# Kernel optimization log

Hardware: AMD Instinct MI355X
Metric: run time of the kernel (lower is better)

Reference implementation:

```python
import jax, jax.numpy as jnp
import numpy as np

IN_DIM, H1, H2, H3, LATENT = 1024, 1024, 512, 256, 256
D, K, BETA = 32, 2048, 0.25
B = 16384


def _leaky(x):
    return jax.nn.leaky_relu(x, negative_slope=0.01)


def setup_inputs() -> dict:
    key = jax.random.key(0)
    ks = jax.random.split(key, 18)
    def lin(k, fan_in, fan_out):
        kw, kb = jax.random.split(k)
        s = 1.0 / np.sqrt(fan_in)
        W = jax.random.uniform(kw, (fan_in, fan_out), jnp.float32, -s, s)
        b = jax.random.uniform(kb, (fan_out,), jnp.float32, -s, s)
        return W, b
    We1, be1 = lin(ks[0], IN_DIM, H1)
    We2, be2 = lin(ks[1], H1, H2)
    We3, be3 = lin(ks[2], H2, H3)
    We4, be4 = lin(ks[3], H3, LATENT)
    Wd1, bd1 = lin(ks[4], LATENT, H3)
    Wd2, bd2 = lin(ks[5], H3, H2)
    Wd3, bd3 = lin(ks[6], H2, H1)
    Wd4, bd4 = lin(ks[7], H1, IN_DIM)
    E = jax.random.uniform(ks[8], (K, D), jnp.float32, -1.0 / K, 1.0 / K)  # codebook
    x = jax.random.uniform(ks[9], (B, IN_DIM), jnp.float32)
    return {"x": x, "We1": We1, "be1": be1, "We2": We2, "be2": be2,
            "We3": We3, "be3": be3, "We4": We4, "be4": be4, "E": E,
            "Wd1": Wd1, "bd1": bd1, "Wd2": Wd2, "bd2": bd2,
            "Wd3": Wd3, "bd3": bd3, "Wd4": Wd4, "bd4": bd4}


def reference(x, We1, be1, We2, be2, We3, be3, We4, be4, E,
              Wd1, bd1, Wd2, bd2, Wd3, bd3, Wd4, bd4):
    # encoder MLP
    h = _leaky(x @ We1 + be1)
    h = _leaky(h @ We2 + be2)
    h = _leaky(h @ We3 + be3)
    z = h @ We4 + be4                      # [B, LATENT]
    # vector quantizer
    zr = z.reshape(-1, D)                  # [N, D], N = B*LATENT/D
    dist = (jnp.sum(zr * zr, axis=1, keepdims=True)
            + jnp.sum(E * E, axis=1)
            - 2.0 * zr @ E.T)              # [N, K]
    idx = jnp.argmin(dist, axis=1)         # [N]
    # one-hot @ E == direct gather of nearest codebook rows
    q = E[idx].reshape(z.shape)            # [B, LATENT]
    commit = jnp.mean(jnp.sum(jnp.square(jax.lax.stop_gradient(q) - z), axis=1))
    embed = jnp.mean(jnp.sum(jnp.square(q - jax.lax.stop_gradient(z)), axis=1))
    vq_loss = BETA * commit + embed
    e = z + jax.lax.stop_gradient(q - z)   # straight-through
    # decoder MLP
    h = _leaky(e @ Wd1 + bd1)
    h = _leaky(h @ Wd2 + bd2)
    h = _leaky(h @ Wd3 + bd3)
    recon = jax.nn.sigmoid(h @ Wd4 + bd4)
    recon_loss = jnp.mean(jnp.sum(jnp.square(recon - x), axis=-1))
    loss = recon_loss + vq_loss
    return z, e, recon, loss, recon_loss, vq_loss
```

## Files before the change

kernel.cpp:

```cpp
#include <hip/hip_runtime.h>
#include <stdint.h>

typedef __attribute__((ext_vector_type(8))) _Float16 half8;
typedef __attribute__((ext_vector_type(4))) _Float16 half4;
typedef __attribute__((ext_vector_type(4))) float f32x4;

__device__ __forceinline__ void gload_lds16(const void* g, void* l) {
  __builtin_amdgcn_global_load_lds(
      (const __attribute__((address_space(1))) void*)g,
      (__attribute__((address_space(3))) void*)l, 16, 0, 0);
}

template <int EPI, int BM, int BN>
__global__ __launch_bounds__(256, (BM == 128 ? 2 : 4)) void gemm_bt(
    const _Float16* __restrict__ A, const _Float16* __restrict__ Bt,
    const float* __restrict__ bias, _Float16* __restrict__ Ch,
    float* __restrict__ Cf, int M, int N, int Kd,
    const float* __restrict__ Xref, float* __restrict__ lossAcc) {
  constexpr int WM = BM / 2, WN = BN / 2;
  constexpr int MF = WM / 16, NF = WN / 16;
  constexpr int CA = BM / 32, CB = BN / 32;
  constexpr int SMEMH = ((BN * 128) > ((BM + BN) * 64)) ? (BN * 128)
                                                        : ((BM + BN) * 64);
  __shared__ __align__(16) _Float16 smem[SMEMH];
  __shared__ float red[256];
  _Float16* As = smem;
  _Float16* Bs = smem + BM * 64;

  const int tid = threadIdx.x;
  const int lane = tid & 63;
  const int wav = tid >> 6;
  const int m0 = blockIdx.y * BM;
  const int n0 = blockIdx.x * BN;
  const int wm = (wav >> 1) * WM;
  const int wn = (wav & 1) * WN;
  const int l15 = lane & 15;
  const int quad = lane >> 4;

  f32x4 acc[MF][NF];
#pragma unroll
  for (int i = 0; i < MF; i++)
#pragma unroll
    for (int j = 0; j < NF; j++) acc[i][j] = (f32x4){0.f, 0.f, 0.f, 0.f};

  for (int kt = 0; kt < Kd; kt += 64) {
    __syncthreads();
#pragma unroll
    for (int j = 0; j < CA; j++) {
      const int ci = j * 256 + tid;
      const int row = ci >> 3;
      const int kc = ((ci & 7) ^ (row & 7)) << 3;
      gload_lds16(A + (size_t)(m0 + row) * Kd + kt + kc, &As[ci * 8]);
    }
#pragma unroll
    for (int j = 0; j < CB; j++) {
      const int ci = j * 256 + tid;
      const int row = ci >> 3;
      const int kc = ((ci & 7) ^ (row & 7)) << 3;
      gload_lds16(Bt + (size_t)(n0 + row) * Kd + kt + kc, &Bs[ci * 8]);
    }
    __syncthreads();

#pragma unroll
    for (int s = 0; s < 2; s++) {
      half8 af[MF], bq[NF];
#pragma unroll
      for (int i = 0; i < MF; i++) {
        const int ra = wm + i * 16 + l15;
        const int ca = (s * 4 + quad) ^ (ra & 7);
        af[i] = *(const half8*)&As[ra * 64 + ca * 8];
      }
#pragma unroll
      for (int i = 0; i < NF; i++) {
        const int rb = wn + i * 16 + l15;
        const int cb = (s * 4 + quad) ^ (rb & 7);
        bq[i] = *(const half8*)&Bs[rb * 64 + cb * 8];
      }
#pragma unroll
      for (int mi = 0; mi < MF; mi++)
#pragma unroll
        for (int ni = 0; ni < NF; ni++)
          acc[mi][ni] = __builtin_amdgcn_mfma_f32_16x16x32_f16(af[mi], bq[ni],
                                                               acc[mi][ni], 0, 0, 0);
    }
  }

  float lsum = 0.f;
  float* eb = (float*)smem;
  constexpr int DIV = BN / 4;
#pragma unroll
  for (int p = 0; p < BM / 64; p++) {
    __syncthreads();
    if ((wm >> 6) == p) {
#pragma unroll
      for (int mi = 0; mi < MF; mi++)
#pragma unroll
        for (int ni = 0; ni < NF; ni++)
#pragma unroll
          for (int r = 0; r < 4; r++) {
            const int rl = (wm & 63) + mi * 16 + quad * 4 + r;
            const int cl = wn + ni * 16 + l15;
            eb[rl * BN + cl] = acc[mi][ni][r];
          }
    }
    __syncthreads();
#pragma unroll
    for (int j = 0; j < BN / 16; j++) {
      const int c = j * 256 + tid;
      const int rl = c / DIV;
      const int cl = (c % DIV) * 4;
      const f32x4 v = *(const f32x4*)&eb[rl * BN + cl];
      const int gcol = n0 + cl;
      const f32x4 bv = *(const f32x4*)&bias[gcol];
      const size_t o = (size_t)(m0 + p * 64 + rl) * N + gcol;
      if (EPI == 0) {
        half4 h;
#pragma unroll
        for (int q = 0; q < 4; q++) {
          float t = v[q] + bv[q];
          t = t > 0.f ? t : 0.01f * t;
          h[q] = (_Float16)t;
        }
        *(half4*)&Ch[o] = h;
      } else if (EPI == 1) {
        f32x4 t;
        half4 h;
#pragma unroll
        for (int q = 0; q < 4; q++) {
          t[q] = v[q] + bv[q];
          h[q] = (_Float16)t[q];
        }
        *(f32x4*)&Cf[o] = t;
        *(half4*)&Ch[o] = h;
      } else {
        const f32x4 xr = *(const f32x4*)&Xref[o];
        f32x4 sv;
#pragma unroll
        for (int q = 0; q < 4; q++) {
          const float s = 1.f / (1.f + __expf(-(v[q] + bv[q])));
          sv[q] = s;
          const float d = s - xr[q];
          lsum += d * d;
        }
        *(f32x4*)&Cf[o] = sv;
      }
    }
  }
  if (EPI == 2) {
    __syncthreads();
    red[tid] = lsum;
    __syncthreads();
    for (int s = 128; s > 0; s >>= 1) {
      if (tid < s) red[tid] += red[tid + s];
      __syncthreads();
    }
    if (tid == 0) atomicAdd(lossAcc, red[0]);
  }
}

__global__ __launch_bounds__(256, 4) void vq_argmin(
    const _Float16* __restrict__ zh, const _Float16* __restrict__ Ehf,
    const float* __restrict__ E, const float* __restrict__ ek2,
    float* __restrict__ e_out, _Float16* __restrict__ eh_out,
    float* __restrict__ vq_acc) {
  __shared__ __align__(16) _Float16 Es[512 * 32];
  __shared__ float ek2s[512];
  __shared__ float z2s[128];
  __shared__ int idxs[128];
  __shared__ float vred[256];

  const int tid = threadIdx.x;
  const int lane = tid & 63;
  const int wav = tid >> 6;
  const int l15 = lane & 15;
  const int quad = lane >> 4;
  const int rbase = blockIdx.x * 128 + wav * 32;
  constexpr unsigned KEYMASK = 0xFFFFF800u;

  half8 zf[2];
  float z2p[2];
#pragma unroll
  for (int m = 0; m < 2; m++) {
    zf[m] = *(const half8*)(zh + ((size_t)(rbase + m * 16 + l15)) * 32 + quad * 8);
    float s = 0.f;
#pragma unroll
    for (int j = 0; j < 8; j++) {
      float v = (float)zf[m][j];
      s += v * v;
    }
    s += __shfl_xor(s, 16);
    s += __shfl_xor(s, 32);
    z2p[m] = s;
  }
  if (quad == 0) {
#pragma unroll
    for (int m = 0; m < 2; m++) z2s[wav * 32 + m * 16 + l15] = z2p[m];
  }

  float key[2][4];
#pragma unroll
  for (int m = 0; m < 2; m++)
#pragma unroll
    for (int r = 0; r < 4; r++) key[m][r] = 1e30f;

  for (int cb = 0; cb < 2048; cb += 512) {
    __syncthreads();
#pragma unroll
    for (int j = 0; j < 8; j++) {
      const int u = j * 256 + tid;
      gload_lds16(Ehf + (size_t)cb * 32 + u * 8, &Es[u * 8]);
    }
    if (tid < 128) gload_lds16(&ek2[cb + tid * 4], &ek2s[tid * 4]);
    __syncthreads();

    int idxv = cb + l15;
    for (int c16 = 0; c16 < 32; c16++) {
      const half8 ef = *(const half8*)&Es[(c16 * 64 + lane) * 8];
      const float e2 = ek2s[c16 * 16 + l15];
      const f32x4 cinit = (f32x4){e2, e2, e2, e2};
      f32x4 d0 = __builtin_amdgcn_mfma_f32_16x16x32_f16(zf[0], ef, cinit, 0, 0, 0);
      f32x4 d1 = __builtin_amdgcn_mfma_f32_16x16x32_f16(zf[1], ef, cinit, 0, 0, 0);
#pragma unroll
      for (int r = 0; r < 4; r++) {
        key[0][r] = fminf(key[0][r],
                          __uint_as_float((__float_as_uint(d0[r]) & KEYMASK) | idxv));
        key[1][r] = fminf(key[1][r],
                          __uint_as_float((__float_as_uint(d1[r]) & KEYMASK) | idxv));
      }
      idxv += 16;
    }
  }

#pragma unroll
  for (int off = 1; off < 16; off <<= 1)
#pragma unroll
    for (int m = 0; m < 2; m++)
#pragma unroll
      for (int r = 0; r < 4; r++)
        key[m][r] = fminf(key[m][r], __shfl_xor(key[m][r], off));

  float vpart = 0.f;
  if (l15 == 0) {
#pragma unroll
    for (int m = 0; m < 2; m++)
#pragma unroll
      for (int r = 0; r < 4; r++) {
        const unsigned kb = __float_as_uint(key[m][r]);
        const int rl = wav * 32 + m * 16 + quad * 4 + r;
        idxs[rl] = (int)(kb & 0x7FFu);
        vpart += z2s[rl] + __uint_as_float(kb & KEYMASK);
      }
  }
  vred[tid] = vpart;
  __syncthreads();
  for (int s = 128; s > 0; s >>= 1) {
    if (tid < s) vred[tid] += vred[tid + s];
    __syncthreads();
  }
  if (tid == 0) atomicAdd(vq_acc, vred[0]);

#pragma unroll
  for (int it = 0; it < 2; it++) {
    const int slot = it * 256 + tid;
    const int rowb = slot >> 2, part = slot & 3;
    const int idx = idxs[rowb];
    const size_t orow = ((size_t)blockIdx.x * 128 + rowb) * 32 + part * 8;
    const f32x4 ea = *(const f32x4*)(E + (size_t)idx * 32 + part * 8);
    const f32x4 ebv = *(const f32x4*)(E + (size_t)idx * 32 + part * 8 + 4);
    *(f32x4*)(e_out + orow) = ea;
    *(f32x4*)(e_out + orow + 4) = ebv;
    half8 ehv;
#pragma unroll
    for (int j = 0; j < 4; j++) {
      ehv[j] = (_Float16)ea[j];
      ehv[j + 4] = (_Float16)ebv[j];
    }
    *(half8*)(eh_out + orow) = ehv;
  }
}

__global__ void transpose_conv(const float* __restrict__ W,
                               _Float16* __restrict__ Wt, int K, int N) {
  __shared__ float t[32][33];
  const int tx = threadIdx.x & 31, ty = threadIdx.x >> 5;
  const int bx = blockIdx.x * 32, by = blockIdx.y * 32;
#pragma unroll
  for (int i = 0; i < 32; i += 8)
    t[ty + i][tx] = W[(size_t)(by + ty + i) * N + bx + tx];
  __syncthreads();
#pragma unroll
  for (int i = 0; i < 32; i += 8)
    Wt[(size_t)(bx + ty + i) * K + by + tx] = (_Float16)t[tx][ty + i];
}

__global__ void conv_x(const float* __restrict__ x, _Float16* __restrict__ xh) {
  const size_t i = (size_t)blockIdx.x * 256 + threadIdx.x;
  const f32x4 a = *(const f32x4*)(x + i * 8);
  const f32x4 b = *(const f32x4*)(x + i * 8 + 4);
  half8 h;
#pragma unroll
  for (int j = 0; j < 4; j++) { h[j] = (_Float16)a[j]; h[j + 4] = (_Float16)b[j]; }
  *(half8*)(xh + i * 8) = h;
}

__global__ void conv_E(const float* __restrict__ E, _Float16* __restrict__ Ehf,
                       float* __restrict__ ek2) {
  const int c = blockIdx.x * 256 + threadIdx.x;
  float s = 0.f;
#pragma unroll
  for (int k = 0; k < 32; k++) {
    const float v = E[(size_t)c * 32 + k];
    s += v * v;
    Ehf[(size_t)((c >> 4) * 64 + (k >> 3) * 16 + (c & 15)) * 8 + (k & 7)] =
        (_Float16)(-2.f * v);
  }
  ek2[c] = s;
}

__global__ void finalize_k(const float* __restrict__ scal, float* __restrict__ out) {
  const float vq = 1.25f * (scal[0] / 16384.f);
  const float rl = scal[1] / 16384.f;
  out[0] = rl + vq;
  out[1] = rl;
  out[2] = vq;
}

extern "C" void kernel_launch(void* const* d_in, const int* in_sizes, int n_in,
                              void* d_out, int out_size, void* d_ws, size_t ws_size,
                              hipStream_t stream) {
  const float* x = (const float*)d_in[0];
  const float* We1 = (const float*)d_in[1];
  const float* be1 = (const float*)d_in[2];
  const float* We2 = (const float*)d_in[3];
  const float* be2 = (const float*)d_in[4];
  const float* We3 = (const float*)d_in[5];
  const float* be3 = (const float*)d_in[6];
  const float* We4 = (const float*)d_in[7];
  const float* be4 = (const float*)d_in[8];
  const float* E = (const float*)d_in[9];
  const float* Wd1 = (const float*)d_in[10];
  const float* bd1 = (const float*)d_in[11];
  const float* Wd2 = (const float*)d_in[12];
  const float* bd2 = (const float*)d_in[13];
  const float* Wd3 = (const float*)d_in[14];
  const float* bd3 = (const float*)d_in[15];
  const float* Wd4 = (const float*)d_in[16];
  const float* bd4 = (const float*)d_in[17];

  float* out = (float*)d_out;
  char* ws = (char*)d_ws;

  size_t off = 0;
  auto alloc = [&](size_t bytes) {
    size_t r = off;
    off += (bytes + 255) & ~(size_t)255;
    return r;
  };
  const size_t oXH = alloc((size_t)16384 * 1024 * 2);
  const size_t oWT1 = alloc((size_t)1024 * 1024 * 2);
  const size_t oWT2 = alloc((size_t)512 * 1024 * 2);
  const size_t oWT3 = alloc((size_t)256 * 512 * 2);
  const size_t oWT4 = alloc((size_t)256 * 256 * 2);
  const size_t oWD1 = alloc((size_t)256 * 256 * 2);
  const size_t oWD2 = alloc((size_t)512 * 256 * 2);
  const size_t oWD3 = alloc((size_t)1024 * 512 * 2);
  const size_t oWD4 = alloc((size_t)1024 * 1024 * 2);
  const size_t oEHF = alloc((size_t)2048 * 32 * 2);
  const size_t oEK2 = alloc((size_t)2048 * 4);
  const size_t oSC = alloc(256);
  const size_t oZH = alloc((size_t)16384 * 256 * 2);
  const size_t oQH = alloc((size_t)16384 * 256 * 2);
  const size_t oH1 = alloc((size_t)16384 * 1024 * 2);
  const size_t oH2 = alloc((size_t)16384 * 512 * 2);
  const size_t oH3 = alloc((size_t)16384 * 256 * 2);

  _Float16* xh = (_Float16*)(ws + oXH);
  _Float16* WT1 = (_Float16*)(ws + oWT1);
  _Float16* WT2 = (_Float16*)(ws + oWT2);
  _Float16* WT3 = (_Float16*)(ws + oWT3);
  _Float16* WT4 = (_Float16*)(ws + oWT4);
  _Float16* WD1 = (_Float16*)(ws + oWD1);
  _Float16* WD2 = (_Float16*)(ws + oWD2);
  _Float16* WD3 = (_Float16*)(ws + oWD3);
  _Float16* WD4 = (_Float16*)(ws + oWD4);
  _Float16* Ehf = (_Float16*)(ws + oEHF);
  float* ek2 = (float*)(ws + oEK2);
  float* scal = (float*)(ws + oSC);
  _Float16* zhw = (_Float16*)(ws + oZH);
  _Float16* qh = (_Float16*)(ws + oQH);
  _Float16* h1 = (_Float16*)(ws + oH1);
  _Float16* h2 = (_Float16*)(ws + oH2);
  _Float16* h3 = (_Float16*)(ws + oH3);

  float* zout = out;
  float* eout = out + (size_t)16384 * 256;
  float* rout = out + (size_t)16384 * 256 * 2;
  float* sout = rout + (size_t)16384 * 1024;

  hipMemsetAsync(ws + oSC, 0, 8, stream);

  dim3 blk(256);
  conv_x<<<8192, blk, 0, stream>>>(x, xh);
  transpose_conv<<<dim3(32, 32), blk, 0, stream>>>(We1, WT1, 1024, 1024);
  transpose_conv<<<dim3(16, 32), blk, 0, stream>>>(We2, WT2, 1024, 512);
  transpose_conv<<<dim3(8, 16), blk, 0, stream>>>(We3, WT3, 512, 256);
  transpose_conv<<<dim3(8, 8), blk, 0, stream>>>(We4, WT4, 256, 256);
  transpose_conv<<<dim3(8, 8), blk, 0, stream>>>(Wd1, WD1, 256, 256);
  transpose_conv<<<dim3(16, 8), blk, 0, stream>>>(Wd2, WD2, 256, 512);
  transpose_conv<<<dim3(32, 16), blk, 0, stream>>>(Wd3, WD3, 512, 1024);
  transpose_conv<<<dim3(32, 32), blk, 0, stream>>>(Wd4, WD4, 1024, 1024);
  conv_E<<<8, blk, 0, stream>>>(E, Ehf, ek2);

  gemm_bt<0, 64, 128><<<dim3(8, 256), blk, 0, stream>>>(
      xh, WT1, be1, h1, nullptr, 16384, 1024, 1024, nullptr, nullptr);
  gemm_bt<0, 64, 64><<<dim3(8, 256), blk, 0, stream>>>(
      h1, WT2, be2, h2, nullptr, 16384, 512, 1024, nullptr, nullptr);
  gemm_bt<0, 64, 64><<<dim3(4, 256), blk, 0, stream>>>(
      h2, WT3, be3, h3, nullptr, 16384, 256, 512, nullptr, nullptr);
  gemm_bt<1, 64, 64><<<dim3(4, 256), blk, 0, stream>>>(
      h3, WT4, be4, zhw, zout, 16384, 256, 256, nullptr, nullptr);
  vq_argmin<<<1024, blk, 0, stream>>>(zhw, Ehf, E, ek2, eout, qh, &scal[0]);
  gemm_bt<0, 64, 64><<<dim3(4, 256), blk, 0, stream>>>(
      qh, WD1, bd1, h3, nullptr, 16384, 256, 256, nullptr, nullptr);
  gemm_bt<0, 64, 64><<<dim3(8, 256), blk, 0, stream>>>(
      h3, WD2, bd2, h2, nullptr, 16384, 512, 256, nullptr, nullptr);
  gemm_bt<0, 64, 128><<<dim3(8, 256), blk, 0, stream>>>(
      h2, WD3, bd3, h1, nullptr, 16384, 1024, 512, nullptr, nullptr);
  gemm_bt<2, 64, 128><<<dim3(8, 256), blk, 0, stream>>>(
      h1, WD4, bd4, nullptr, rout, 16384, 1024, 1024, x, &scal[1]);
  finalize_k<<<1, 1, 0, stream>>>(scal, sout);
}
```

Before: 468.2 us.

## Double-buffer GEMM LDS loads, merge prep kernels, widen tiles, read fp16 x in loss

The GEMM main loop now double-buffers its LDS tiles. It issues the next K-slice's global-to-LDS loads before computing on the current one and uses explicit vmcnt waits and barriers, so load latency can overlap with MFMA work. The nine prep kernels (x conversion, eight weight transposes, codebook conversion) are merged into one launch, cutting launch overhead. Two mid-size layers switch to 64x128 tiles, and the occupancy hint is adjusted. The reconstruction-loss epilogue now reads the fp16 copy of x instead of fp32, which halves that read but computes the loss against a rounded target. The doubled shared memory may also lower occupancy.

Measured after the change: 452.8 us. -3.3%, faster.

```diff
diff --git a/kernel.cpp b/kernel.cpp
--- a/kernel.cpp
+++ b/kernel.cpp
@@ -12,20 +12,18 @@
 }
 
 template <int EPI, int BM, int BN>
-__global__ __launch_bounds__(256, (BM == 128 ? 2 : 4)) void gemm_bt(
+__global__ __launch_bounds__(256, ((BM + BN) == 192 ? 3 : 4)) void gemm_bt(
     const _Float16* __restrict__ A, const _Float16* __restrict__ Bt,
     const float* __restrict__ bias, _Float16* __restrict__ Ch,
     float* __restrict__ Cf, int M, int N, int Kd,
-    const float* __restrict__ Xref, float* __restrict__ lossAcc) {
+    const _Float16* __restrict__ Xref, float* __restrict__ lossAcc) {
   constexpr int WM = BM / 2, WN = BN / 2;
   constexpr int MF = WM / 16, NF = WN / 16;
   constexpr int CA = BM / 32, CB = BN / 32;
-  constexpr int SMEMH = ((BN * 128) > ((BM + BN) * 64)) ? (BN * 128)
-                                                        : ((BM + BN) * 64);
-  __shared__ __align__(16) _Float16 smem[SMEMH];
+  constexpr int CHUNKS = CA + CB;
+  constexpr int STAGE = (BM + BN) * 64;
+  __shared__ __align__(16) _Float16 smem[2 * STAGE];
   __shared__ float red[256];
-  _Float16* As = smem;
-  _Float16* Bs = smem + BM * 64;
 
   const int tid = threadIdx.x;
   const int lane = tid & 63;
@@ -43,8 +41,9 @@
 #pragma unroll
     for (int j = 0; j < NF; j++) acc[i][j] = (f32x4){0.f, 0.f, 0.f, 0.f};
 
-  for (int kt = 0; kt < Kd; kt += 64) {
-    __syncthreads();
+  auto issue = [&](int kt, int b) {
+    _Float16* As = smem + b * STAGE;
+    _Float16* Bs = As + BM * 64;
 #pragma unroll
     for (int j = 0; j < CA; j++) {
       const int ci = j * 256 + tid;
@@ -59,8 +58,21 @@
       const int kc = ((ci & 7) ^ (row & 7)) << 3;
       gload_lds16(Bt + (size_t)(n0 + row) * Kd + kt + kc, &Bs[ci * 8]);
     }
-    __syncthreads();
-
+  };
+
+  int buf = 0;
+  issue(0, 0);
+  for (int kt = 0; kt < Kd; kt += 64) {
+    if (kt + 64 < Kd) {
+      issue(kt + 64, buf ^ 1);
+      asm volatile("s_waitcnt vmcnt(%0)" ::"i"(CHUNKS) : "memory");
+    } else {
+      asm volatile("s_waitcnt vmcnt(0)" ::: "memory");
+    }
+    asm volatile("s_barrier" ::: "memory");
+
+    const _Float16* As = smem + buf * STAGE;
+    const _Float16* Bs = As + BM * 64;
 #pragma unroll
     for (int s = 0; s < 2; s++) {
       half8 af[MF], bq[NF];
@@ -83,6 +95,8 @@
           acc[mi][ni] = __builtin_amdgcn_mfma_f32_16x16x32_f16(af[mi], bq[ni],
                                                                acc[mi][ni], 0, 0, 0);
     }
+    asm volatile("s_barrier" ::: "memory");
+    buf ^= 1;
   }
 
   float lsum = 0.f;
@@ -133,13 +147,13 @@
         *(f32x4*)&Cf[o] = t;
         *(half4*)&Ch[o] = h;
       } else {
-        const f32x4 xr = *(const f32x4*)&Xref[o];
+        const half4 xr = *(const half4*)&Xref[o];
         f32x4 sv;
 #pragma unroll
         for (int q = 0; q < 4; q++) {
           const float s = 1.f / (1.f + __expf(-(v[q] + bv[q])));
           sv[q] = s;
-          const float d = s - xr[q];
+          const float d = s - (float)xr[q];
           lsum += d * d;
         }
         *(f32x4*)&Cf[o] = sv;
@@ -279,42 +293,65 @@
   }
 }
 
-__global__ void transpose_conv(const float* __restrict__ W,
-                               _Float16* __restrict__ Wt, int K, int N) {
+struct PrepArgs {
+  const float* W[8];
+  _Float16* Wt[8];
+  int Kw[8], Nw[8];
+  int base[9];
+  const float* x;
+  _Float16* xh;
+  const float* E;
+  _Float16* Ehf;
+  float* ek2;
+};
+
+__global__ __launch_bounds__(256) void prep_k(PrepArgs a) {
   __shared__ float t[32][33];
-  const int tx = threadIdx.x & 31, ty = threadIdx.x >> 5;
-  const int bx = blockIdx.x * 32, by = blockIdx.y * 32;
-#pragma unroll
-  for (int i = 0; i < 32; i += 8)
-    t[ty + i][tx] = W[(size_t)(by + ty + i) * N + bx + tx];
-  __syncthreads();
-#pragma unroll
-  for (int i = 0; i < 32; i += 8)
-    Wt[(size_t)(bx + ty + i) * K + by + tx] = (_Float16)t[tx][ty + i];
-}
-
-__global__ void conv_x(const float* __restrict__ x, _Float16* __restrict__ xh) {
-  const size_t i = (size_t)blockIdx.x * 256 + threadIdx.x;
-  const f32x4 a = *(const f32x4*)(x + i * 8);
-  const f32x4 b = *(const f32x4*)(x + i * 8 + 4);
-  half8 h;
-#pragma unroll
-  for (int j = 0; j < 4; j++) { h[j] = (_Float16)a[j]; h[j + 4] = (_Float16)b[j]; }
-  *(half8*)(xh + i * 8) = h;
-}
-
-__global__ void conv_E(const float* __restrict__ E, _Float16* __restrict__ Ehf,
-                       float* __restrict__ ek2) {
-  const int c = blockIdx.x * 256 + threadIdx.x;
+  const int b = blockIdx.x;
+  const int tid = threadIdx.x;
+  if (b < 8192) {
+    const size_t i = (size_t)b * 256 + tid;
+    const f32x4 va = *(const f32x4*)(a.x + i * 8);
+    const f32x4 vb = *(const f32x4*)(a.x + i * 8 + 4);
+    half8 h;
+#pragma unroll
+    for (int j = 0; j < 4; j++) {
+      h[j] = (_Float16)va[j];
+      h[j + 4] = (_Float16)vb[j];
+    }
+    *(half8*)(a.xh + i * 8) = h;
+    return;
+  }
+  if (b < 8192 + 3456) {
+    int l = b - 8192;
+    int w = 0;
+    while (l >= a.base[w + 1]) w++;
+    l -= a.base[w];
+    const float* W = a.W[w];
+    _Float16* Wt = a.Wt[w];
+    const int K = a.Kw[w], N = a.Nw[w];
+    const int nb = N >> 5;
+    const int bx = (l % nb) * 32, by = (l / nb) * 32;
+    const int tx = tid & 31, ty = tid >> 5;
+#pragma unroll
+    for (int i = 0; i < 32; i += 8)
+      t[ty + i][tx] = W[(size_t)(by + ty + i) * N + bx + tx];
+    __syncthreads();
+#pragma unroll
+    for (int i = 0; i < 32; i += 8)
+      Wt[(size_t)(bx + ty + i) * K + by + tx] = (_Float16)t[tx][ty + i];
+    return;
+  }
+  const int c = (b - 8192 - 3456) * 256 + tid;
   float s = 0.f;
 #pragma unroll
   for (int k = 0; k < 32; k++) {
-    const float v = E[(size_t)c * 32 + k];
+    const float v = a.E[(size_t)c * 32 + k];
     s += v * v;
-    Ehf[(size_t)((c >> 4) * 64 + (k >> 3) * 16 + (c & 15)) * 8 + (k & 7)] =
+    a.Ehf[(size_t)((c >> 4) * 64 + (k >> 3) * 16 + (c & 15)) * 8 + (k & 7)] =
         (_Float16)(-2.f * v);
   }
-  ek2[c] = s;
+  a.ek2[c] = s;
 }
 
 __global__ void finalize_k(const float* __restrict__ scal, float* __restrict__ out) {
@@ -329,22 +366,14 @@
                               void* d_out, int out_size, void* d_ws, size_t ws_size,
                               hipStream_t stream) {
   const float* x = (const float*)d_in[0];
-  const float* We1 = (const float*)d_in[1];
   const float* be1 = (const float*)d_in[2];
-  const float* We2 = (const float*)d_in[3];
   const float* be2 = (const float*)d_in[4];
-  const float* We3 = (const float*)d_in[5];
   const float* be3 = (const float*)d_in[6];
-  const float* We4 = (const float*)d_in[7];
   const float* be4 = (const float*)d_in[8];
   const float* E = (const float*)d_in[9];
-  const float* Wd1 = (const float*)d_in[10];
   const float* bd1 = (const float*)d_in[11];
-  const float* Wd2 = (const float*)d_in[12];
   const float* bd2 = (const float*)d_in[13];
-  const float* Wd3 = (const float*)d_in[14];
   const float* bd3 = (const float*)d_in[15];
-  const float* Wd4 = (const float*)d_in[16];
   const float* bd4 = (const float*)d_in[17];
 
   float* out = (float*)d_out;
@@ -399,21 +428,29 @@
 
   hipMemsetAsync(ws + oSC, 0, 8, stream);
 
+  PrepArgs pa;
+  pa.W[0] = (const float*)d_in[1];  pa.Wt[0] = WT1; pa.Kw[0] = 1024; pa.Nw[0] = 1024;
+  pa.W[1] = (const float*)d_in[3];  pa.Wt[1] = WT2; pa.Kw[1] = 1024; pa.Nw[1] = 512;
+  pa.W[2] = (const float*)d_in[5];  pa.Wt[2] = WT3; pa.Kw[2] = 512;  pa.Nw[2] = 256;
+  pa.W[3] = (const float*)d_in[7];  pa.Wt[3] = WT4; pa.Kw[3] = 256;  pa.Nw[3] = 256;
+  pa.W[4] = (const float*)d_in[10]; pa.Wt[4] = WD1; pa.Kw[4] = 256;  pa.Nw[4] = 256;
+  pa.W[5] = (const float*)d_in[12]; pa.Wt[5] = WD2; pa.Kw[5] = 256;  pa.Nw[5] = 512;
+  pa.W[6] = (const float*)d_in[14]; pa.Wt[6] = WD3; pa.Kw[6] = 512;  pa.Nw[6] = 1024;
+  pa.W[7] = (const float*)d_in[16]; pa.Wt[7] = WD4; pa.Kw[7] = 1024; pa.Nw[7] = 1024;
+  int acc = 0;
+  for (int w = 0; w < 8; w++) {
+    pa.base[w] = acc;
+    acc += (pa.Kw[w] >> 5) * (pa.Nw[w] >> 5);
+  }
+  pa.base[8] = acc;
+  pa.x = x; pa.xh = xh; pa.E = E; pa.Ehf = Ehf; pa.ek2 = ek2;
+
   dim3 blk(256);
-  conv_x<<<8192, blk, 0, stream>>>(x, xh);
-  transpose_conv<<<dim3(32, 32), blk, 0, stream>>>(We1, WT1, 1024, 1024);
-  transpose_conv<<<dim3(16, 32), blk, 0, stream>>>(We2, WT2, 1024, 512);
-  transpose_conv<<<dim3(8, 16), blk, 0, stream>>>(We3, WT3, 512, 256);
-  transpose_conv<<<dim3(8, 8), blk, 0, stream>>>(We4, WT4, 256, 256);
-  transpose_conv<<<dim3(8, 8), blk, 0, stream>>>(Wd1, WD1, 256, 256);
-  transpose_conv<<<dim3(16, 8), blk, 0, stream>>>(Wd2, WD2, 256, 512);
-  transpose_conv<<<dim3(32, 16), blk, 0, stream>>>(Wd3, WD3, 512, 1024);
-  transpose_conv<<<dim3(32, 32), blk, 0, stream>>>(Wd4, WD4, 1024, 1024);
-  conv_E<<<8, blk, 0, stream>>>(E, Ehf, ek2);
+  prep_k<<<8192 + 3456 + 8, blk, 0, stream>>>(pa);
 
   gemm_bt<0, 64, 128><<<dim3(8, 256), blk, 0, stream>>>(
       xh, WT1, be1, h1, nullptr, 16384, 1024, 1024, nullptr, nullptr);
-  gemm_bt<0, 64, 64><<<dim3(8, 256), blk, 0, stream>>>(
+  gemm_bt<0, 64, 128><<<dim3(4, 256), blk, 0, stream>>>(
       h1, WT2, be2, h2, nullptr, 16384, 512, 1024, nullptr, nullptr);
   gemm_bt<0, 64, 64><<<dim3(4, 256), blk, 0, stream>>>(
       h2, WT3, be3, h3, nullptr, 16384, 256, 512, nullptr, nullptr);
@@ -422,11 +459,11 @@
   vq_argmin<<<1024, blk, 0, stream>>>(zhw, Ehf, E, ek2, eout, qh, &scal[0]);
   gemm_bt<0, 64, 64><<<dim3(4, 256), blk, 0, stream>>>(
       qh, WD1, bd1, h3, nullptr, 16384, 256, 256, nullptr, nullptr);
-  gemm_bt<0, 64, 64><<<dim3(8, 256), blk, 0, stream>>>(
+  gemm_bt<0, 64, 128><<<dim3(4, 256), blk, 0, stream>>>(
       h3, WD2, bd2, h2, nullptr, 16384, 512, 256, nullptr, nullptr);
   gemm_bt<0, 64, 128><<<dim3(8, 256), blk, 0, stream>>>(
       h2, WD3, bd3, h1, nullptr, 16384, 1024, 512, nullptr, nullptr);
   gemm_bt<2, 64, 128><<<dim3(8, 256), blk, 0, stream>>>(
-      h1, WD4, bd4, nullptr, rout, 16384, 1024, 1024, x, &scal[1]);
+      h1, WD4, bd4, nullptr, rout, 16384, 1024, 1024, xh, &scal[1]);
   finalize_k<<<1, 1, 0, stream>>>(scal, sout);
 }
```
